# Optimization experiments

Hardware: AMD Instinct MI355X
Metric: run time of the kernel (lower is better)

## Reference

```python
import jax, jax.numpy as jnp
import numpy as np

B, T = 1024, 8192


def setup_inputs() -> dict:
    key = jax.random.key(0)
    k1, k2 = jax.random.split(key)
    # phi/psi are [B, T, 2] probability-bound robustness traces in [0, 1]
    phi = jax.random.uniform(k1, (B, T, 2), dtype=jnp.float32)
    psi = jax.random.uniform(k2, (B, T, 2), dtype=jnp.float32)
    return {"phi": phi, "psi": psi}


def reference(phi, psi):
    """Until operator, interval [0, inf), exact (scale<=0) min/max.

    Original O(T^2) double loop computes, for each t:
        out[t] = max_{tau in [t, T-1]} min( min(phi[t..tau-1]), psi[tau] )
    with the empty segment (tau == t) contributing min(ones, psi[t]).
    Because min distributes over max, this satisfies the exact O(T)
    backward recurrence:
        r[t] = max( min(1, psi[t]), min(phi[t], r[t+1]) ),  r[T] = -inf
    which we evaluate with a reversed lax.scan over the time axis.
    """
    phi_t = jnp.swapaxes(phi, 0, 1)  # [T, B, 2]
    psi_t = jnp.swapaxes(psi, 0, 1)  # [T, B, 2]

    def step(carry, xs):
        p, q = xs
        v = jnp.minimum(jnp.asarray(1.0, p.dtype), q)  # tau == t term (min with ones)
        r = jnp.maximum(v, jnp.minimum(p, carry))
        return r, r

    init = jnp.full(phi_t.shape[1:], -jnp.inf, dtype=phi.dtype)  # [B, 2]
    _, out = jax.lax.scan(step, init, (phi_t, psi_t), reverse=True)
    return jnp.swapaxes(out, 0, 1)  # [B, T, 2]
```

## Files before the change

### kernel.cpp

```cpp
#include <hip/hip_runtime.h>
#include <math.h>


#define T_LEN 8192
#define NSEG  8
#define BLOCK (NSEG * 64)

__device__ __forceinline__ float rfl(float x) {
    return __int_as_float(__builtin_amdgcn_readfirstlane(__float_as_int(x)));
}

__global__ __launch_bounds__(BLOCK) void until_kernel(
    const float* __restrict__ phi, const float* __restrict__ psi,
    float* __restrict__ out)
{
    const int row  = blockIdx.x;
    const int tid  = threadIdx.x;
    const int w    = tid >> 6;
    const int lane = tid & 63;

    const float NEG = -__builtin_huge_valf();
    const float POS =  __builtin_huge_valf();

    const size_t segf4 = (size_t)row * (T_LEN / 2) + (size_t)w * 512;
    const float4* __restrict__ phi4 = (const float4*)phi + segf4;
    const float4* __restrict__ psi4 = (const float4*)psi + segf4;
    float4* __restrict__ out4 = (float4*)out + segf4;

    __shared__ float4 ssum[NSEG];

    float runAx = NEG, runAy = NEG, runBx = POS, runBy = POS;
#pragma unroll
    for (int k = 0; k < 8; ++k) {
        float4 P = phi4[k * 64 + lane];
        float4 Q = psi4[k * 64 + lane];
        float v0x = fminf(1.f, Q.x), v0y = fminf(1.f, Q.y);
        float v1x = fminf(1.f, Q.z), v1y = fminf(1.f, Q.w);
        float Gax = fmaxf(v0x, fminf(P.x, v1x));
        float Gay = fmaxf(v0y, fminf(P.y, v1y));
        float Gbx = fminf(P.x, P.z);
        float Gby = fminf(P.y, P.w);
#pragma unroll
        for (int off = 1; off < 64; off <<= 1) {
            float gax = __shfl_down(Gax, off), gay = __shfl_down(Gay, off);
            float gbx = __shfl_down(Gbx, off), gby = __shfl_down(Gby, off);
            bool val = (lane + off) < 64;
            gax = val ? gax : NEG;  gay = val ? gay : NEG;
            gbx = val ? gbx : POS;  gby = val ? gby : POS;
            Gax = fmaxf(Gax, fminf(Gbx, gax));
            Gay = fmaxf(Gay, fminf(Gby, gay));
            Gbx = fminf(Gbx, gbx);
            Gby = fminf(Gby, gby);
        }
        float cax = rfl(Gax), cay = rfl(Gay), cbx = rfl(Gbx), cby = rfl(Gby);
        runAx = fmaxf(runAx, fminf(runBx, cax));
        runAy = fmaxf(runAy, fminf(runBy, cay));
        runBx = fminf(runBx, cbx);
        runBy = fminf(runBy, cby);
    }
    if (lane == 0) ssum[w] = make_float4(runAx, runAy, runBx, runBy);
    __syncthreads();

    float rex = NEG, rey = NEG;
    for (int j = NSEG - 1; j > w; --j) {
        float4 s = ssum[j];
        rex = fmaxf(s.x, fminf(s.z, rex));
        rey = fmaxf(s.y, fminf(s.w, rey));
    }

#pragma unroll
    for (int k = 7; k >= 0; --k) {
        float4 P = phi4[k * 64 + lane];
        float4 Q = psi4[k * 64 + lane];
        float v0x = fminf(1.f, Q.x), v0y = fminf(1.f, Q.y);
        float v1x = fminf(1.f, Q.z), v1y = fminf(1.f, Q.w);
        float Gax = fmaxf(v0x, fminf(P.x, v1x));
        float Gay = fmaxf(v0y, fminf(P.y, v1y));
        float Gbx = fminf(P.x, P.z);
        float Gby = fminf(P.y, P.w);
#pragma unroll
        for (int off = 1; off < 64; off <<= 1) {
            float gax = __shfl_down(Gax, off), gay = __shfl_down(Gay, off);
            float gbx = __shfl_down(Gbx, off), gby = __shfl_down(Gby, off);
            bool val = (lane + off) < 64;
            gax = val ? gax : NEG;  gay = val ? gay : NEG;
            gbx = val ? gbx : POS;  gby = val ? gby : POS;
            Gax = fmaxf(Gax, fminf(Gbx, gax));
            Gay = fmaxf(Gay, fminf(Gby, gay));
            Gbx = fminf(Gbx, gbx);
            Gby = fminf(Gby, gby);
        }
        float yx = fmaxf(Gax, fminf(Gbx, rex));
        float yy = fmaxf(Gay, fminf(Gby, rey));
        float ynx = __shfl_down(yx, 1), yny = __shfl_down(yy, 1);
        if (lane == 63) { ynx = rex; yny = rey; }
        float r1x = fmaxf(v1x, fminf(P.z, ynx));
        float r1y = fmaxf(v1y, fminf(P.w, yny));
        float r0x = fmaxf(v0x, fminf(P.x, r1x));
        float r0y = fmaxf(v0y, fminf(P.y, r1y));
        out4[k * 64 + lane] = make_float4(r0x, r0y, r1x, r1y);
        rex = rfl(yx);
        rey = rfl(yy);
    }
}

extern "C" void kernel_launch(void* const* d_in, const int* in_sizes, int n_in,
                              void* d_out, int out_size, void* d_ws, size_t ws_size,
                              hipStream_t stream) {
    const float* phi = (const float*)d_in[0];
    const float* psi = (const float*)d_in[1];
    float* out = (float*)d_out;
    const int Bn = in_sizes[0] / (T_LEN * 2);
    until_kernel<<<Bn, BLOCK, 0, stream>>>(phi, psi, out);
}
```

Before: 186.6 us.

## Transpose pair summaries through LDS to scan 4 elements per lane before shuffles

Result: faster. 181.6 us (-2.7%).

```diff
diff --git a/kernel.cpp b/kernel.cpp
--- a/kernel.cpp
+++ b/kernel.cpp
@@ -1,5 +1,4 @@
 #include <hip/hip_runtime.h>
-#include <math.h>
 
 
 #define T_LEN 8192
@@ -14,11 +13,10 @@
     const float* __restrict__ phi, const float* __restrict__ psi,
     float* __restrict__ out)
 {
-    const int row  = blockIdx.x;
-    const int tid  = threadIdx.x;
-    const int w    = tid >> 6;
-    const int lane = tid & 63;
-
+    const int  row  = blockIdx.x;
+    const int  tid  = threadIdx.x;
+    const int  w    = tid >> 6;
+    const int  lane = tid & 63;
     const float NEG = -__builtin_huge_valf();
     const float POS =  __builtin_huge_valf();
 
@@ -27,80 +25,121 @@
     const float4* __restrict__ psi4 = (const float4*)psi + segf4;
     float4* __restrict__ out4 = (float4*)out + segf4;
 
+    __shared__ alignas(16) float lds[NSEG * 1024];
     __shared__ float4 ssum[NSEG];
+    float* wl = lds + w * 1024;
 
-    float runAx = NEG, runAy = NEG, runBx = POS, runBy = POS;
+    float4 GAx[2], GAy[2], GBx[2], GBy[2];
+    float  Sax[2], Say[2], Sbx[2], Sby[2];
+
+#pragma unroll
+    for (int r = 0; r < 2; ++r) {
+#pragma unroll
+        for (int kl = 0; kl < 4; ++kl) {
+            const int e  = (r * 4 + kl) * 64 + lane;
+            const int El = kl * 64 + lane;
+            float4 P = phi4[e];
+            float4 Q = psi4[e];
+            float v0x = fminf(1.f, Q.x), v0y = fminf(1.f, Q.y);
+            float v1x = fminf(1.f, Q.z), v1y = fminf(1.f, Q.w);
+            wl[0 * 256 + El] = fmaxf(v0x, fminf(P.x, v1x));
+            wl[1 * 256 + El] = fmaxf(v0y, fminf(P.y, v1y));
+            wl[2 * 256 + El] = fminf(P.x, P.z);
+            wl[3 * 256 + El] = fminf(P.y, P.w);
+        }
+        __syncthreads();
+        GAx[r] = *(const float4*)(wl + 0 * 256 + lane * 4);
+        GAy[r] = *(const float4*)(wl + 1 * 256 + lane * 4);
+        GBx[r] = *(const float4*)(wl + 2 * 256 + lane * 4);
+        GBy[r] = *(const float4*)(wl + 3 * 256 + lane * 4);
+        __syncthreads();
+
+        float hax = GAx[r].w, hay = GAy[r].w, hbx = GBx[r].w, hby = GBy[r].w;
+        hax = fmaxf(GAx[r].z, fminf(GBx[r].z, hax));
+        hay = fmaxf(GAy[r].z, fminf(GBy[r].z, hay));
+        hbx = fminf(GBx[r].z, hbx);
+        hby = fminf(GBy[r].z, hby);
+        hax = fmaxf(GAx[r].y, fminf(GBx[r].y, hax));
+        hay = fmaxf(GAy[r].y, fminf(GBy[r].y, hay));
+        hbx = fminf(GBx[r].y, hbx);
+        hby = fminf(GBy[r].y, hby);
+        hax = fmaxf(GAx[r].x, fminf(GBx[r].x, hax));
+        hay = fmaxf(GAy[r].x, fminf(GBy[r].x, hay));
+        hbx = fminf(GBx[r].x, hbx);
+        hby = fminf(GBy[r].x, hby);
+
+#pragma unroll
+        for (int off = 1; off < 64; off <<= 1) {
+            float gax = __shfl_down(hax, off), gay = __shfl_down(hay, off);
+            float gbx = __shfl_down(hbx, off), gby = __shfl_down(hby, off);
+            bool  val = (lane + off) < 64;
+            gax = val ? gax : NEG;  gay = val ? gay : NEG;
+            gbx = val ? gbx : POS;  gby = val ? gby : POS;
+            hax = fmaxf(hax, fminf(hbx, gax));
+            hay = fmaxf(hay, fminf(hby, gay));
+            hbx = fminf(hbx, gbx);
+            hby = fminf(hby, gby);
+        }
+        Sax[r] = hax; Say[r] = hay; Sbx[r] = hbx; Sby[r] = hby;
+    }
+
+    float R0ax = rfl(Sax[0]), R0ay = rfl(Say[0]);
+    float R0bx = rfl(Sbx[0]), R0by = rfl(Sby[0]);
+    float R1ax = rfl(Sax[1]), R1ay = rfl(Say[1]);
+    float R1bx = rfl(Sbx[1]), R1by = rfl(Sby[1]);
+    if (lane == 0) {
+        float wax = fmaxf(R0ax, fminf(R0bx, R1ax));
+        float way = fmaxf(R0ay, fminf(R0by, R1ay));
+        float wbx = fminf(R0bx, R1bx);
+        float wby = fminf(R0by, R1by);
+        ssum[w] = make_float4(wax, way, wbx, wby);
+    }
+    __syncthreads();
+    float rcx = NEG, rcy = NEG;
+    for (int j = NSEG - 1; j > w; --j) {
+        float4 s = ssum[j];
+        rcx = fmaxf(s.x, fminf(s.z, rcx));
+        rcy = fmaxf(s.y, fminf(s.w, rcy));
+    }
+
+    float rinx[2], riny[2];
+    rinx[1] = rcx;
+    riny[1] = rcy;
+    rinx[0] = fmaxf(R1ax, fminf(R1bx, rcx));
+    riny[0] = fmaxf(R1ay, fminf(R1by, rcy));
+
+#pragma unroll
+    for (int r = 0; r < 2; ++r) {
+        float yx = fmaxf(Sax[r], fminf(Sbx[r], rinx[r]));
+        float yy = fmaxf(Say[r], fminf(Sby[r], riny[r]));
+        float cx = __shfl_down(yx, 1), cy = __shfl_down(yy, 1);
+        if (lane == 63) { cx = rinx[r]; cy = riny[r]; }
+        float4 CX, CY;
+        CX.w = cx;
+        CY.w = cy;
+        CX.z = fmaxf(GAx[r].w, fminf(GBx[r].w, CX.w));
+        CY.z = fmaxf(GAy[r].w, fminf(GBy[r].w, CY.w));
+        CX.y = fmaxf(GAx[r].z, fminf(GBx[r].z, CX.z));
+        CY.y = fmaxf(GAy[r].z, fminf(GBy[r].z, CY.z));
+        CX.x = fmaxf(GAx[r].y, fminf(GBx[r].y, CX.y));
+        CY.x = fmaxf(GAy[r].y, fminf(GBy[r].y, CY.y));
+        *(float4*)(wl +       r * 256 + lane * 4) = CX;
+        *(float4*)(wl + 512 + r * 256 + lane * 4) = CY;
+    }
+    __syncthreads();
+
 #pragma unroll
     for (int k = 0; k < 8; ++k) {
-        float4 P = phi4[k * 64 + lane];
-        float4 Q = psi4[k * 64 + lane];
-        float v0x = fminf(1.f, Q.x), v0y = fminf(1.f, Q.y);
-        float v1x = fminf(1.f, Q.z), v1y = fminf(1.f, Q.w);
-        float Gax = fmaxf(v0x, fminf(P.x, v1x));
-        float Gay = fmaxf(v0y, fminf(P.y, v1y));
-        float Gbx = fminf(P.x, P.z);
-        float Gby = fminf(P.y, P.w);
-#pragma unroll
-        for (int off = 1; off < 64; off <<= 1) {
-            float gax = __shfl_down(Gax, off), gay = __shfl_down(Gay, off);
-            float gbx = __shfl_down(Gbx, off), gby = __shfl_down(Gby, off);
-            bool val = (lane + off) < 64;
-            gax = val ? gax : NEG;  gay = val ? gay : NEG;
-            gbx = val ? gbx : POS;  gby = val ? gby : POS;
-            Gax = fmaxf(Gax, fminf(Gbx, gax));
-            Gay = fmaxf(Gay, fminf(Gby, gay));
-            Gbx = fminf(Gbx, gbx);
-            Gby = fminf(Gby, gby);
-        }
-        float cax = rfl(Gax), cay = rfl(Gay), cbx = rfl(Gbx), cby = rfl(Gby);
-        runAx = fmaxf(runAx, fminf(runBx, cax));
-        runAy = fmaxf(runAy, fminf(runBy, cay));
-        runBx = fminf(runBx, cbx);
-        runBy = fminf(runBy, cby);
-    }
-    if (lane == 0) ssum[w] = make_float4(runAx, runAy, runBx, runBy);
-    __syncthreads();
-
-    float rex = NEG, rey = NEG;
-    for (int j = NSEG - 1; j > w; --j) {
-        float4 s = ssum[j];
-        rex = fmaxf(s.x, fminf(s.z, rex));
-        rey = fmaxf(s.y, fminf(s.w, rey));
-    }
-
-#pragma unroll
-    for (int k = 7; k >= 0; --k) {
-        float4 P = phi4[k * 64 + lane];
-        float4 Q = psi4[k * 64 + lane];
-        float v0x = fminf(1.f, Q.x), v0y = fminf(1.f, Q.y);
-        float v1x = fminf(1.f, Q.z), v1y = fminf(1.f, Q.w);
-        float Gax = fmaxf(v0x, fminf(P.x, v1x));
-        float Gay = fmaxf(v0y, fminf(P.y, v1y));
-        float Gbx = fminf(P.x, P.z);
-        float Gby = fminf(P.y, P.w);
-#pragma unroll
-        for (int off = 1; off < 64; off <<= 1) {
-            float gax = __shfl_down(Gax, off), gay = __shfl_down(Gay, off);
-            float gbx = __shfl_down(Gbx, off), gby = __shfl_down(Gby, off);
-            bool val = (lane + off) < 64;
-            gax = val ? gax : NEG;  gay = val ? gay : NEG;
-            gbx = val ? gbx : POS;  gby = val ? gby : POS;
-            Gax = fmaxf(Gax, fminf(Gbx, gax));
-            Gay = fmaxf(Gay, fminf(Gby, gay));
-            Gbx = fminf(Gbx, gbx);
-            Gby = fminf(Gby, gby);
-        }
-        float yx = fmaxf(Gax, fminf(Gbx, rex));
-        float yy = fmaxf(Gay, fminf(Gby, rey));
-        float ynx = __shfl_down(yx, 1), yny = __shfl_down(yy, 1);
-        if (lane == 63) { ynx = rex; yny = rey; }
-        float r1x = fmaxf(v1x, fminf(P.z, ynx));
-        float r1y = fmaxf(v1y, fminf(P.w, yny));
-        float r0x = fmaxf(v0x, fminf(P.x, r1x));
-        float r0y = fmaxf(v0y, fminf(P.y, r1y));
-        out4[k * 64 + lane] = make_float4(r0x, r0y, r1x, r1y);
-        rex = rfl(yx);
-        rey = rfl(yy);
+        const int e = k * 64 + lane;
+        float4 P = phi4[e];
+        float4 Q = psi4[e];
+        float cx = wl[e];
+        float cy = wl[512 + e];
+        float r1x = fmaxf(fminf(1.f, Q.z), fminf(P.z, cx));
+        float r1y = fmaxf(fminf(1.f, Q.w), fminf(P.w, cy));
+        float r0x = fmaxf(fminf(1.f, Q.x), fminf(P.x, r1x));
+        float r0y = fmaxf(fminf(1.f, Q.y), fminf(P.y, r1y));
+        out4[e] = make_float4(r0x, r0y, r1x, r1y);
     }
 }
 
```
